# Kernel tuning notes

Hardware: AMD Instinct MI355X
Metric: run time of the kernel (lower is better)

## Reference

```python
import jax, jax.numpy as jnp
import numpy as np

GRID_SIZE = 64
SPLINE_ORDER = 3
NUM_BASIS = GRID_SIZE + SPLINE_ORDER - 1  # 66
GRID_MIN, GRID_MAX = -1.0, 1.0
EPS = 1e-7
B, IN_F, OUT_F = 4096, 256, 256


def setup_inputs() -> dict:
    key = jax.random.key(0)
    k1, k2, k3, k4 = jax.random.split(key, 4)
    x = jax.random.normal(k1, (B, IN_F), dtype=jnp.float32)
    base_weight = jax.random.normal(k2, (IN_F, OUT_F), dtype=jnp.float32) * (1.0 / np.sqrt(IN_F))
    scale = 1.0 / np.sqrt(NUM_BASIS)
    spline_weight = jax.random.uniform(k3, (IN_F, OUT_F, NUM_BASIS), dtype=jnp.float32, minval=-scale, maxval=scale)
    spline_scaler = jax.random.uniform(k4, (IN_F, OUT_F), dtype=jnp.float32)
    return {"x": x, "base_weight": base_weight, "spline_weight": spline_weight, "spline_scaler": spline_scaler}


def _spline_basis(x):
    # normalize to [0,1], map onto grid coordinate
    x_c = jnp.clip(x, GRID_MIN, GRID_MAX)
    x_norm = (x_c - GRID_MIN) / (GRID_MAX - GRID_MIN + EPS)
    x_scaled = x_norm * (GRID_SIZE - 1)
    grid_idx = jnp.clip(jnp.floor(x_scaled), 0.0, GRID_SIZE - SPLINE_ORDER)
    local_x = x_scaled - grid_idx                                  # [B, in]
    centers = jnp.linspace(0.0, 1.0, NUM_BASIS, dtype=jnp.float32)  # [nb]
    sigma = 1.0 / NUM_BASIS
    bv = jnp.exp(-jnp.square(local_x[..., None] - centers) / (2.0 * sigma * sigma))  # [B, in, nb]
    # (safe_mode clip is skipped at inference: training falsy)
    bv = bv / (jnp.sum(bv, axis=-1, keepdims=True) + EPS)
    return bv


def reference(x, base_weight, spline_weight, spline_scaler):
    base_out = x @ base_weight                                     # [B, out]
    basis = _spline_basis(x)                                       # [B, in, nb]
    # sum over basis then over in_features: same math as the expanded
    # elementwise-product/sum chain in the original call()
    spline_out = jnp.einsum('bik,iok->bo', basis, spline_weight)   # [B, out]
    scaling = jnp.mean(jnp.maximum(spline_scaler, EPS), axis=0)    # [out]
    return base_out + spline_out * scaling
```

## Files before the change

### kernel.cpp

```cpp
#include <hip/hip_runtime.h>
#include <stdint.h>


#define IN_F 256
#define OUT_F 256
#define NB 66
#define KP 80
#define APAD 88
#define KSPLIT 8
#define SLABS 32
#define BM 128
#define NTHREADS 512

typedef __attribute__((ext_vector_type(8))) short bf16x8;
typedef __attribute__((ext_vector_type(16))) float f32x16;

__device__ __forceinline__ unsigned int f2bf(float f) {
  unsigned int u = __float_as_uint(f);
  u += 0x7FFFu + ((u >> 16) & 1u);
  return u >> 16;
}

__global__ void kan_scale8(const float* __restrict__ sca, float* __restrict__ wsp) {
  const int o = threadIdx.x, b = blockIdx.x;
  float s = 0.0f;
  #pragma unroll
  for (int j = 0; j < 32; j++) {
    const int i = b * 32 + j;
    s += fmaxf(sca[(size_t)i * OUT_F + o], 1e-7f);
  }
  wsp[b * OUT_F + o] = s;
}

__global__ void kan_pack(const float* __restrict__ sw, const float* __restrict__ bw,
                         const float* __restrict__ wsp, unsigned short* __restrict__ wp2) {
  const int i = blockIdx.x, o = threadIdx.x;
  float sc = 0.0f;
  #pragma unroll
  for (int b = 0; b < 8; b++) sc += wsp[b * OUT_F + o];
  sc *= (1.0f / 256.0f);
  const float2* src = (const float2*)(sw + ((size_t)i * OUT_F + o) * NB);
  float v[80];
  #pragma unroll
  for (int j = 0; j < 33; j++) {
    float2 t2 = src[j];
    v[2 * j] = t2.x * sc;
    v[2 * j + 1] = t2.y * sc;
  }
  v[66] = bw[(size_t)i * OUT_F + o];
  #pragma unroll
  for (int k = 67; k < 80; k++) v[k] = 0.0f;
  uint4* dst = (uint4*)wp2;
  #pragma unroll
  for (int g = 0; g < 10; g++) {
    uint4 u;
    unsigned int* up = (unsigned int*)&u;
    #pragma unroll
    for (int h = 0; h < 4; h++)
      up[h] = f2bf(v[g * 8 + 2 * h]) | (f2bf(v[g * 8 + 2 * h + 1]) << 16);
    dst[((size_t)i * 10 + g) * OUT_F + o] = u;
  }
}

__global__ __launch_bounds__(NTHREADS, 2) void kan_main(
    const float* __restrict__ x, const unsigned short* __restrict__ wp2,
    float* __restrict__ dst, int atomic_mode) {
  __shared__ unsigned short A[2][BM * APAD];

  const int t = threadIdx.x;
  const int lane = t & 63;
  const int w = t >> 6;
  const int ml = lane & 31;
  const int half = lane >> 5;
  const int mr = w >> 2;
  const int nc = w & 3;
  const int mblk = (int)blockIdx.x >> 3;
  const int kidx = (int)blockIdx.x & 7;
  const int b0 = mblk * BM;
  const int ibase = kidx * SLABS;

  const int rb = t >> 2;
  const int q = t & 3;
  const int ks = (q == 0) ? 0 : (q == 1) ? 24 : (q == 2) ? 40 : 64;
  const int len = (q & 1) ? 16 : 24;
  const int nchunk = len >> 3;

  const float* xrow = x + (size_t)(b0 + rb) * IN_F;
  const int boff = (nc * 64 + ml) * 8;

  bf16x8 breg[2][10];
  f32x16 acc[4] = {f32x16{}, f32x16{}, f32x16{}, f32x16{}};

#define LOADB(P, ISLAB)                                                        \
  {                                                                            \
    const unsigned short* bp =                                                 \
        wp2 + (size_t)(ISLAB) * (OUT_F * KP) + half * 2048 + boff;             \
    _Pragma("unroll") for (int kk = 0; kk < 5; kk++) {                         \
      breg[P][kk] = *(const bf16x8*)(bp + kk * 4096);                          \
      breg[P][5 + kk] = *(const bf16x8*)(bp + kk * 4096 + 256);                \
    }                                                                          \
  }

#define BASIS(BUFSEL, XVAL)                                                    \
  {                                                                            \
    const float xr_ = (XVAL);                                                  \
    const float xc_ = fminf(fmaxf(xr_, -1.0f), 1.0f);                          \
    const float xs_ = (xc_ + 1.0f) * (63.0f / (2.0f + 1e-7f));                 \
    const float tl_ = xs_ - fminf(floorf(xs_), 61.0f);                         \
    float e_[24];                                                              \
    float s_ = 0.0f;                                                           \
    _Pragma("unroll") for (int j = 0; j < 24; j++) {                           \
      const int k = ks + j;                                                    \
      const float d_ = tl_ - (float)k * (1.0f / 65.0f);                        \
      float ee = __expf(-2178.0f * d_ * d_);                                   \
      ee = (j < len && k < 66) ? ee : 0.0f;                                    \
      e_[j] = ee;                                                              \
      s_ += ee;                                                                \
    }                                                                          \
    s_ += __shfl_xor(s_, 1);                                                   \
    s_ += __shfl_xor(s_, 2);                                                   \
    const float r_ = __fdividef(1.0f, s_ + 1e-7f);                             \
    unsigned short* Ar = &A[BUFSEL][rb * APAD + ks];                           \
    _Pragma("unroll") for (int c = 0; c < 3; c++) {                            \
      if (c < nchunk) {                                                        \
        uint4 u;                                                               \
        unsigned int* up = (unsigned int*)&u;                                  \
        _Pragma("unroll") for (int h = 0; h < 4; h++) {                        \
          const int k0 = ks + c * 8 + h * 2;                                   \
          float f0 = e_[c * 8 + h * 2] * r_;                                   \
          float f1 = e_[c * 8 + h * 2 + 1] * r_;                               \
          f0 = (k0 == 66) ? xr_ : f0;                                          \
          f1 = (k0 + 1 == 66) ? xr_ : f1;                                      \
          up[h] = f2bf(f0) | (f2bf(f1) << 16);                                 \
        }                                                                      \
        *(uint4*)(Ar + c * 8) = u;                                             \
      }                                                                        \
    }                                                                          \
  }

#define MFMA_SLAB(CUR, P)                                                      \
  {                                                                            \
    const unsigned short* Ac = &A[CUR][0];                                     \
    _Pragma("unroll") for (int kk = 0; kk < 5; kk++) {                         \
      const int ko = kk * 16 + half * 8;                                       \
      bf16x8 a0 = *(const bf16x8*)(Ac + (mr * 64 + ml) * APAD + ko);           \
      bf16x8 a1 = *(const bf16x8*)(Ac + (mr * 64 + 32 + ml) * APAD + ko);      \
      acc[0] = __builtin_amdgcn_mfma_f32_32x32x16_bf16(a0, breg[P][kk], acc[0], 0, 0, 0);       \
      acc[1] = __builtin_amdgcn_mfma_f32_32x32x16_bf16(a0, breg[P][5 + kk], acc[1], 0, 0, 0);   \
      acc[2] = __builtin_amdgcn_mfma_f32_32x32x16_bf16(a1, breg[P][kk], acc[2], 0, 0, 0);       \
      acc[3] = __builtin_amdgcn_mfma_f32_32x32x16_bf16(a1, breg[P][5 + kk], acc[3], 0, 0, 0);   \
    }                                                                          \
  }

  BASIS(0, xrow[ibase]);
  LOADB(0, ibase);
  float xn = xrow[ibase + 1];
  __syncthreads();

#define STEP(II, P)                                                            \
  {                                                                            \
    if ((II) + 1 < SLABS) LOADB(1 - (P), ibase + (II) + 1);                    \
    MFMA_SLAB((II) & 1, P);                                                    \
    const float xc2 = xn;                                                      \
    if ((II) + 2 < SLABS) xn = xrow[ibase + (II) + 2];                         \
    if ((II) + 1 < SLABS) BASIS(((II) + 1) & 1, xc2);                          \
    __syncthreads();                                                           \
  }

  for (int ii = 0; ii < SLABS; ii += 2) {
    STEP(ii, 0);
    STEP(ii + 1, 1);
  }

  const int colb = nc * 64 + ml;
  if (atomic_mode) {
    #pragma unroll
    for (int mb = 0; mb < 2; mb++) {
      #pragma unroll
      for (int r = 0; r < 16; r++) {
        const int row = b0 + mr * 64 + mb * 32 + (r & 3) + 8 * (r >> 2) + 4 * half;
        atomicAdd(&dst[(size_t)row * OUT_F + colb], acc[mb * 2][r]);
        atomicAdd(&dst[(size_t)row * OUT_F + colb + 32], acc[mb * 2 + 1][r]);
      }
    }
  } else {
    float* pd = dst + (size_t)kidx * ((size_t)4096 * OUT_F);
    #pragma unroll
    for (int mb = 0; mb < 2; mb++) {
      #pragma unroll
      for (int r = 0; r < 16; r++) {
        const int row = b0 + mr * 64 + mb * 32 + (r & 3) + 8 * (r >> 2) + 4 * half;
        pd[(size_t)row * OUT_F + colb] = acc[mb * 2][r];
        pd[(size_t)row * OUT_F + colb + 32] = acc[mb * 2 + 1][r];
      }
    }
  }
}

__global__ void kan_reduce(const float* __restrict__ part, float* __restrict__ out) {
  const size_t j = ((size_t)blockIdx.x * 256 + threadIdx.x) * 4;
  float4 a = *(const float4*)(part + j);
  #pragma unroll
  for (int s = 1; s < 8; s++) {
    float4 b = *(const float4*)(part + (size_t)s * 1048576 + j);
    a.x += b.x; a.y += b.y; a.z += b.z; a.w += b.w;
  }
  *(float4*)(out + j) = a;
}

__global__ void kan_naive(const float* __restrict__ x, const float* __restrict__ bw,
                          const float* __restrict__ sw, const float* __restrict__ sca,
                          float* __restrict__ out) {
  const int o = threadIdx.x;
  const int b = blockIdx.x;
  float accb = 0.0f, accs = 0.0f, scl = 0.0f;
  for (int i = 0; i < IN_F; i++) {
    const float xraw = x[(size_t)b * IN_F + i];
    accb += xraw * bw[(size_t)i * OUT_F + o];
    scl += fmaxf(sca[(size_t)i * OUT_F + o], 1e-7f);
    const float xc = fminf(fmaxf(xraw, -1.0f), 1.0f);
    const float xs = (xc + 1.0f) * (63.0f / (2.0f + 1e-7f));
    const float tl = xs - fminf(floorf(xs), 61.0f);
    const int kc = (int)(tl * 65.0f + 0.5f);
    const int k0 = max(0, min(kc - 8, 50));
    float e[16]; float s = 0.0f;
    #pragma unroll
    for (int j = 0; j < 16; j++) {
      float d = tl - (float)(k0 + j) * (1.0f / 65.0f);
      e[j] = __expf(-2178.0f * d * d);
      s += e[j];
    }
    const float r = __fdividef(1.0f, s + 1e-7f);
    const float* wrow = sw + ((size_t)i * OUT_F + o) * NB + k0;
    float dot = 0.0f;
    #pragma unroll
    for (int j = 0; j < 16; j++) dot += e[j] * wrow[j];
    accs += dot * r;
  }
  out[(size_t)b * OUT_F + o] = accb + accs * (scl * (1.0f / 256.0f));
}

extern "C" void kernel_launch(void* const* d_in, const int* in_sizes, int n_in,
                              void* d_out, int out_size, void* d_ws, size_t ws_size,
                              hipStream_t stream) {
  const float* x   = (const float*)d_in[0];
  const float* bw  = (const float*)d_in[1];
  const float* sw  = (const float*)d_in[2];
  const float* sca = (const float*)d_in[3];
  float* out = (float*)d_out;

  const size_t WP2_BYTES  = (size_t)IN_F * OUT_F * KP * 2;
  const size_t WP_OFF     = 8192;
  const size_t PART_OFF   = WP_OFF + WP2_BYTES;
  const size_t PART_BYTES = (size_t)KSPLIT * 4096 * OUT_F * 4;

  if (ws_size >= PART_OFF + PART_BYTES) {
    float* wsp = (float*)d_ws;
    unsigned short* wp2 = (unsigned short*)((char*)d_ws + WP_OFF);
    float* part = (float*)((char*)d_ws + PART_OFF);
    kan_scale8<<<8, 256, 0, stream>>>(sca, wsp);
    kan_pack<<<256, 256, 0, stream>>>(sw, bw, wsp, wp2);
    kan_main<<<256, NTHREADS, 0, stream>>>(x, wp2, part, 0);
    kan_reduce<<<1024, 256, 0, stream>>>(part, out);
  } else if (ws_size >= PART_OFF) {
    float* wsp = (float*)d_ws;
    unsigned short* wp2 = (unsigned short*)((char*)d_ws + WP_OFF);
    hipMemsetAsync(d_out, 0, (size_t)out_size * sizeof(float), stream);
    kan_scale8<<<8, 256, 0, stream>>>(sca, wsp);
    kan_pack<<<256, 256, 0, stream>>>(sw, bw, wsp, wp2);
    kan_main<<<256, NTHREADS, 0, stream>>>(x, wp2, out, 1);
  } else {
    kan_naive<<<4096, 256, 0, stream>>>(x, bw, sw, sca, out);
  }
}
```

Before: 155.5 us.

## Halve row tile to 64 and remap waves to 32-column strips

Shrinks the batch tile from 128 to 64 rows and doubles the grid to 512 blocks. Each of the 8 waves now owns a 32-column strip across all 64 rows, and the basis computation is split across 8 threads per row instead of 4. Fewer accumulators and B registers let launch bounds allow 4 blocks per CU, aiming for better occupancy and CU coverage. In exchange each B slab is loaded by twice as many blocks, and every wave reuses its B fragments across fewer rows.

```diff
diff --git a/kernel.cpp b/kernel.cpp
--- a/kernel.cpp
+++ b/kernel.cpp
@@ -9,8 +9,9 @@
 #define APAD 88
 #define KSPLIT 8
 #define SLABS 32
-#define BM 128
+#define BM 64
 #define NTHREADS 512
+#define GRID_MAIN 512
 
 typedef __attribute__((ext_vector_type(8))) short bf16x8;
 typedef __attribute__((ext_vector_type(16))) float f32x16;
@@ -62,7 +63,7 @@
   }
 }
 
-__global__ __launch_bounds__(NTHREADS, 2) void kan_main(
+__global__ __launch_bounds__(NTHREADS, 4) void kan_main(
     const float* __restrict__ x, const unsigned short* __restrict__ wp2,
     float* __restrict__ dst, int atomic_mode) {
   __shared__ unsigned short A[2][BM * APAD];
@@ -72,24 +73,22 @@
   const int w = t >> 6;
   const int ml = lane & 31;
   const int half = lane >> 5;
-  const int mr = w >> 2;
-  const int nc = w & 3;
   const int mblk = (int)blockIdx.x >> 3;
   const int kidx = (int)blockIdx.x & 7;
   const int b0 = mblk * BM;
   const int ibase = kidx * SLABS;
 
-  const int rb = t >> 2;
-  const int q = t & 3;
-  const int ks = (q == 0) ? 0 : (q == 1) ? 24 : (q == 2) ? 40 : 64;
-  const int len = (q & 1) ? 16 : 24;
+  const int rb = t >> 3;
+  const int q = t & 7;
+  const int ks = (q + (q > 0) + (q > 4)) * 8;
+  const int len = ((q & 3) == 0) ? 16 : 8;
   const int nchunk = len >> 3;
 
   const float* xrow = x + (size_t)(b0 + rb) * IN_F;
-  const int boff = (nc * 64 + ml) * 8;
-
-  bf16x8 breg[2][10];
-  f32x16 acc[4] = {f32x16{}, f32x16{}, f32x16{}, f32x16{}};
+  const int boff = (w * 32 + ml) * 8;
+
+  bf16x8 breg[2][5];
+  f32x16 acc[2] = {f32x16{}, f32x16{}};
 
 #define LOADB(P, ISLAB)                                                        \
   {                                                                            \
@@ -97,7 +96,6 @@
         wp2 + (size_t)(ISLAB) * (OUT_F * KP) + half * 2048 + boff;             \
     _Pragma("unroll") for (int kk = 0; kk < 5; kk++) {                         \
       breg[P][kk] = *(const bf16x8*)(bp + kk * 4096);                          \
-      breg[P][5 + kk] = *(const bf16x8*)(bp + kk * 4096 + 256);                \
     }                                                                          \
   }
 
@@ -107,9 +105,9 @@
     const float xc_ = fminf(fmaxf(xr_, -1.0f), 1.0f);                          \
     const float xs_ = (xc_ + 1.0f) * (63.0f / (2.0f + 1e-7f));                 \
     const float tl_ = xs_ - fminf(floorf(xs_), 61.0f);                         \
-    float e_[24];                                                              \
+    float e_[16];                                                              \
     float s_ = 0.0f;                                                           \
-    _Pragma("unroll") for (int j = 0; j < 24; j++) {                           \
+    _Pragma("unroll") for (int j = 0; j < 16; j++) {                           \
       const int k = ks + j;                                                    \
       const float d_ = tl_ - (float)k * (1.0f / 65.0f);                        \
       float ee = __expf(-2178.0f * d_ * d_);                                   \
@@ -119,9 +117,10 @@
     }                                                                          \
     s_ += __shfl_xor(s_, 1);                                                   \
     s_ += __shfl_xor(s_, 2);                                                   \
+    s_ += __shfl_xor(s_, 4);                                                   \
     const float r_ = __fdividef(1.0f, s_ + 1e-7f);                             \
     unsigned short* Ar = &A[BUFSEL][rb * APAD + ks];                           \
-    _Pragma("unroll") for (int c = 0; c < 3; c++) {                            \
+    _Pragma("unroll") for (int c = 0; c < 2; c++) {                            \
       if (c < nchunk) {                                                        \
         uint4 u;                                                               \
         unsigned int* up = (unsigned int*)&u;                                  \
@@ -143,12 +142,10 @@
     const unsigned short* Ac = &A[CUR][0];                                     \
     _Pragma("unroll") for (int kk = 0; kk < 5; kk++) {                         \
       const int ko = kk * 16 + half * 8;                                       \
-      bf16x8 a0 = *(const bf16x8*)(Ac + (mr * 64 + ml) * APAD + ko);           \
-      bf16x8 a1 = *(const bf16x8*)(Ac + (mr * 64 + 32 + ml) * APAD + ko);      \
-      acc[0] = __builtin_amdgcn_mfma_f32_32x32x16_bf16(a0, breg[P][kk], acc[0], 0, 0, 0);       \
-      acc[1] = __builtin_amdgcn_mfma_f32_32x32x16_bf16(a0, breg[P][5 + kk], acc[1], 0, 0, 0);   \
-      acc[2] = __builtin_amdgcn_mfma_f32_32x32x16_bf16(a1, breg[P][kk], acc[2], 0, 0, 0);       \
-      acc[3] = __builtin_amdgcn_mfma_f32_32x32x16_bf16(a1, breg[P][5 + kk], acc[3], 0, 0, 0);   \
+      bf16x8 a0 = *(const bf16x8*)(Ac + ml * APAD + ko);                       \
+      bf16x8 a1 = *(const bf16x8*)(Ac + (32 + ml) * APAD + ko);                \
+      acc[0] = __builtin_amdgcn_mfma_f32_32x32x16_bf16(a0, breg[P][kk], acc[0], 0, 0, 0); \
+      acc[1] = __builtin_amdgcn_mfma_f32_32x32x16_bf16(a1, breg[P][kk], acc[1], 0, 0, 0); \
     }                                                                          \
   }
 
@@ -172,15 +169,14 @@
     STEP(ii + 1, 1);
   }
 
-  const int colb = nc * 64 + ml;
+  const int colb = w * 32 + ml;
   if (atomic_mode) {
     #pragma unroll
     for (int mb = 0; mb < 2; mb++) {
       #pragma unroll
       for (int r = 0; r < 16; r++) {
-        const int row = b0 + mr * 64 + mb * 32 + (r & 3) + 8 * (r >> 2) + 4 * half;
-        atomicAdd(&dst[(size_t)row * OUT_F + colb], acc[mb * 2][r]);
-        atomicAdd(&dst[(size_t)row * OUT_F + colb + 32], acc[mb * 2 + 1][r]);
+        const int row = b0 + mb * 32 + (r & 3) + 8 * (r >> 2) + 4 * half;
+        atomicAdd(&dst[(size_t)row * OUT_F + colb], acc[mb][r]);
       }
     }
   } else {
@@ -189,9 +185,8 @@
     for (int mb = 0; mb < 2; mb++) {
       #pragma unroll
       for (int r = 0; r < 16; r++) {
-        const int row = b0 + mr * 64 + mb * 32 + (r & 3) + 8 * (r >> 2) + 4 * half;
-        pd[(size_t)row * OUT_F + colb] = acc[mb * 2][r];
-        pd[(size_t)row * OUT_F + colb + 32] = acc[mb * 2 + 1][r];
+        const int row = b0 + mb * 32 + (r & 3) + 8 * (r >> 2) + 4 * half;
+        pd[(size_t)row * OUT_F + colb] = acc[mb][r];
       }
     }
   }
@@ -260,7 +255,7 @@
     float* part = (float*)((char*)d_ws + PART_OFF);
     kan_scale8<<<8, 256, 0, stream>>>(sca, wsp);
     kan_pack<<<256, 256, 0, stream>>>(sw, bw, wsp, wp2);
-    kan_main<<<256, NTHREADS, 0, stream>>>(x, wp2, part, 0);
+    kan_main<<<GRID_MAIN, NTHREADS, 0, stream>>>(x, wp2, part, 0);
     kan_reduce<<<1024, 256, 0, stream>>>(part, out);
   } else if (ws_size >= PART_OFF) {
     float* wsp = (float*)d_ws;
@@ -268,7 +263,7 @@
     hipMemsetAsync(d_out, 0, (size_t)out_size * sizeof(float), stream);
     kan_scale8<<<8, 256, 0, stream>>>(sca, wsp);
     kan_pack<<<256, 256, 0, stream>>>(sw, bw, wsp, wp2);
-    kan_main<<<256, NTHREADS, 0, stream>>>(x, wp2, out, 1);
+    kan_main<<<GRID_MAIN, NTHREADS, 0, stream>>>(x, wp2, out, 1);
   } else {
     kan_naive<<<4096, 256, 0, stream>>>(x, bw, sw, sca, out);
   }
```

Measured after the change: 157.6 us. About the same (+1.4%).
